# Optimization experiments

Hardware: AMD Instinct MI355X
Metric: run time of the kernel (lower is better)

Reference implementation:

```python
import jax, jax.numpy as jnp
import numpy as np
from jax import lax

T, D, NH, CATS = 1024, 2048, 2048, 1000


def setup_inputs() -> dict:
    key = jax.random.key(0)
    ks = jax.random.split(key, 16)
    s = 0.02
    return {
        "x": jax.random.normal(ks[0], (T, D), dtype=jnp.float32),
        "Wh": jax.random.normal(ks[1], (NH, D), dtype=jnp.float32) * s,
        "Wz": jax.random.normal(ks[2], (NH, D), dtype=jnp.float32) * s,
        "Wr": jax.random.normal(ks[3], (NH, D), dtype=jnp.float32) * s,
        "Uh": jax.random.normal(ks[4], (NH, NH), dtype=jnp.float32) * s,
        "Uz": jax.random.normal(ks[5], (NH, NH), dtype=jnp.float32) * s,
        "bz": jax.random.normal(ks[6], (NH,), dtype=jnp.float32) * s,
        "Ur": jax.random.normal(ks[7], (NH, NH), dtype=jnp.float32) * s,
        "br": jax.random.normal(ks[8], (NH,), dtype=jnp.float32) * s,
        "Wout": jax.random.normal(ks[9], (CATS, NH), dtype=jnp.float32) * s,
        "h0": jax.random.normal(ks[10], (NH,), dtype=jnp.float32),
        "zt0": jax.random.normal(ks[11], (NH,), dtype=jnp.float32),
        "htilde0": jax.random.normal(ks[12], (NH,), dtype=jnp.float32),
        "hprev0": jax.random.normal(ks[13], (NH,), dtype=jnp.float32),
    }


def reference(x, Wh, Wz, Wr, Uh, Uz, bz, Ur, br, Wout, h0, zt0, htilde0, hprev0):
    # Batch the input projections over all timesteps: [T,d] @ [d,nh] -> [T,nh]
    xh = x @ Wh.T
    xz = x @ Wz.T
    xr = x @ Wr.T

    # Faithful to the original update ORDER: h is computed from the *stale*
    # zt/htilde (from the previous iteration), then gates are refreshed.
    # The original's hadamard(a, b) = linear(a, diag(b)) is exactly a * b.
    def step(carry, xs):
        h, zt, htilde, hprev = carry
        xh_t, xz_t, xr_t = xs
        h_new = (1.0 - zt) * hprev + zt * htilde
        zt_new = jax.nn.sigmoid(xz_t + hprev @ Uz.T + bz)
        htilde_new = jnp.tanh(xh_t + hprev @ Uh.T)
        # rt = sigmoid(xr_t + hprev @ Ur.T + br)  # computed in original, never used
        return (h_new, zt_new, htilde_new, h_new), None

    (h_fin, _, _, _), _ = lax.scan(step, (h0, zt0, htilde0, hprev0), (xh, xz, xr))
    logits = h_fin @ Wout.T  # [cats]
    return jax.nn.softmax(logits, axis=0)
```

## Files before the change

### kernel.cpp

```cpp
#include <hip/hip_runtime.h>
#include <math.h>

#define TT  1024
#define DD  2048
#define NHH 2048
#define CC  1000

__global__ __launch_bounds__(256) void k_gemm(const float* __restrict__ X,
                                              const float* __restrict__ Wh,
                                              const float* __restrict__ Wz,
                                              const float* __restrict__ bz,
                                              float* __restrict__ XH,
                                              float* __restrict__ XZ) {
    __shared__ float As[32][68];
    __shared__ float Bs[32][68];
    const int z = blockIdx.z;
    const float* __restrict__ W = z ? Wz : Wh;
    float* __restrict__ OUT = z ? XZ : XH;
    const int n0 = blockIdx.x * 64;
    const int m0 = blockIdx.y * 64;
    const int tid = threadIdx.x;
    const int tx = tid & 15, ty = tid >> 4;
    const int lr = tid >> 2;
    const int lc = (tid & 3) * 8;

    float acc[4][4] = {};
    for (int k0 = 0; k0 < DD; k0 += 32) {
        float4 a0 = *(const float4*)&X[(size_t)(m0 + lr) * DD + k0 + lc];
        float4 a1 = *(const float4*)&X[(size_t)(m0 + lr) * DD + k0 + lc + 4];
        float4 b0 = *(const float4*)&W[(size_t)(n0 + lr) * DD + k0 + lc];
        float4 b1 = *(const float4*)&W[(size_t)(n0 + lr) * DD + k0 + lc + 4];
        As[lc+0][lr]=a0.x; As[lc+1][lr]=a0.y; As[lc+2][lr]=a0.z; As[lc+3][lr]=a0.w;
        As[lc+4][lr]=a1.x; As[lc+5][lr]=a1.y; As[lc+6][lr]=a1.z; As[lc+7][lr]=a1.w;
        Bs[lc+0][lr]=b0.x; Bs[lc+1][lr]=b0.y; Bs[lc+2][lr]=b0.z; Bs[lc+3][lr]=b0.w;
        Bs[lc+4][lr]=b1.x; Bs[lc+5][lr]=b1.y; Bs[lc+6][lr]=b1.z; Bs[lc+7][lr]=b1.w;
        __syncthreads();
#pragma unroll
        for (int kk = 0; kk < 32; ++kk) {
            float4 av = *(const float4*)&As[kk][ty * 4];
            float4 bv = *(const float4*)&Bs[kk][tx * 4];
            acc[0][0] = fmaf(av.x, bv.x, acc[0][0]); acc[0][1] = fmaf(av.x, bv.y, acc[0][1]);
            acc[0][2] = fmaf(av.x, bv.z, acc[0][2]); acc[0][3] = fmaf(av.x, bv.w, acc[0][3]);
            acc[1][0] = fmaf(av.y, bv.x, acc[1][0]); acc[1][1] = fmaf(av.y, bv.y, acc[1][1]);
            acc[1][2] = fmaf(av.y, bv.z, acc[1][2]); acc[1][3] = fmaf(av.y, bv.w, acc[1][3]);
            acc[2][0] = fmaf(av.z, bv.x, acc[2][0]); acc[2][1] = fmaf(av.z, bv.y, acc[2][1]);
            acc[2][2] = fmaf(av.z, bv.z, acc[2][2]); acc[2][3] = fmaf(av.z, bv.w, acc[2][3]);
            acc[3][0] = fmaf(av.w, bv.x, acc[3][0]); acc[3][1] = fmaf(av.w, bv.y, acc[3][1]);
            acc[3][2] = fmaf(av.w, bv.z, acc[3][2]); acc[3][3] = fmaf(av.w, bv.w, acc[3][3]);
        }
        __syncthreads();
    }
    float4 bias = make_float4(0.f, 0.f, 0.f, 0.f);
    if (z) bias = *(const float4*)&bz[n0 + tx * 4];
#pragma unroll
    for (int i = 0; i < 4; ++i) {
        float4 o = make_float4(acc[i][0] + bias.x, acc[i][1] + bias.y,
                               acc[i][2] + bias.z, acc[i][3] + bias.w);
        *(float4*)&OUT[(size_t)(m0 + ty * 4 + i) * NHH + n0 + tx * 4] = o;
    }
}

__global__ __launch_bounds__(256, 1) void k_recur(
    const float* __restrict__ XH, const float* __restrict__ XZ,
    const float* __restrict__ Uh, const float* __restrict__ Uz,
    const float* __restrict__ zt0, const float* __restrict__ ht0,
    const float* __restrict__ hp0,
    unsigned long long* __restrict__ Hbuf) {
    __shared__ float Hs[NHH];
    __shared__ float dot_s[16];
    const int tid  = threadIdx.x;
    const int wave = tid >> 6, lane = tid & 63;
    const int base8 = blockIdx.x * 8;

    const float* __restrict__ Um = (wave < 2) ? Uz : Uh;
    const int r0 = base8 + (wave & 1) * 4;
    float u[4][32];
#pragma unroll
    for (int r = 0; r < 4; ++r) {
        const float* __restrict__ row = Um + (size_t)(r0 + r) * NHH;
#pragma unroll
        for (int c = 0; c < 8; ++c) {
            float4 v = *(const float4*)&row[c * 256 + lane * 4];
            u[r][c*4+0] = v.x; u[r][c*4+1] = v.y; u[r][c*4+2] = v.z; u[r][c*4+3] = v.w;
        }
    }
#pragma unroll
    for (int k = 0; k < 8; ++k) Hs[k * 256 + tid] = hp0[k * 256 + tid];

    float p_cur = 0.f;
    if (tid < 8) {
        float z0 = zt0[base8 + tid], g0 = ht0[base8 + tid], p0 = hp0[base8 + tid];
        p_cur = (1.0f - z0) * p0 + z0 * g0;
        unsigned long long pr = (1ull << 32) | (unsigned long long)__float_as_uint(p_cur);
        __hip_atomic_store(&Hbuf[(size_t)1 * NHH + base8 + tid], pr,
                           __ATOMIC_RELAXED, __HIP_MEMORY_SCOPE_AGENT);
    }
    __syncthreads();

    for (int t = 1; t < TT; ++t) {
        const unsigned long long* __restrict__ src = Hbuf + (size_t)(t & 3) * NHH;
        unsigned long long pv[8];
#pragma unroll
        for (int k = 0; k < 8; ++k)
            pv[k] = __hip_atomic_load(&src[k * 256 + tid], __ATOMIC_RELAXED, __HIP_MEMORY_SCOPE_AGENT);
        float xzv = 0.f, xhv = 0.f;
        if (tid < 8) {
            xzv = XZ[(size_t)(t - 1) * NHH + base8 + tid];
            xhv = XH[(size_t)(t - 1) * NHH + base8 + tid];
        }
        float a0 = 0.f, a1 = 0.f, a2 = 0.f, a3 = 0.f;
#pragma unroll
        for (int c = 0; c < 8; ++c) {
            float4 h4 = *(const float4*)&Hs[c * 256 + lane * 4];
            a0 = fmaf(u[0][c*4+0], h4.x, fmaf(u[0][c*4+1], h4.y, fmaf(u[0][c*4+2], h4.z, fmaf(u[0][c*4+3], h4.w, a0))));
            a1 = fmaf(u[1][c*4+0], h4.x, fmaf(u[1][c*4+1], h4.y, fmaf(u[1][c*4+2], h4.z, fmaf(u[1][c*4+3], h4.w, a1))));
            a2 = fmaf(u[2][c*4+0], h4.x, fmaf(u[2][c*4+1], h4.y, fmaf(u[2][c*4+2], h4.z, fmaf(u[2][c*4+3], h4.w, a2))));
            a3 = fmaf(u[3][c*4+0], h4.x, fmaf(u[3][c*4+1], h4.y, fmaf(u[3][c*4+2], h4.z, fmaf(u[3][c*4+3], h4.w, a3))));
        }
#pragma unroll
        for (int off = 32; off > 0; off >>= 1) {
            a0 += __shfl_xor(a0, off);
            a1 += __shfl_xor(a1, off);
            a2 += __shfl_xor(a2, off);
            a3 += __shfl_xor(a3, off);
        }
        if (lane == 0) {
            int di = ((wave & 1) * 4) + ((wave >> 1) * 8);
            dot_s[di + 0] = a0; dot_s[di + 1] = a1; dot_s[di + 2] = a2; dot_s[di + 3] = a3;
        }
        __syncthreads();
        if (tid < 8) {
            float z = 1.0f / (1.0f + expf(-(xzv + dot_s[tid])));
            float g = tanhf(xhv + dot_s[8 + tid]);
            float pn = (1.0f - z) * p_cur + z * g;
            p_cur = pn;
            unsigned long long pr = ((unsigned long long)(unsigned)(t + 1) << 32)
                                  | (unsigned long long)__float_as_uint(pn);
            __hip_atomic_store(&Hbuf[(size_t)((t + 1) & 3) * NHH + base8 + tid], pr,
                               __ATOMIC_RELAXED, __HIP_MEMORY_SCOPE_AGENT);
        }
        for (;;) {
            unsigned stale = 0;
#pragma unroll
            for (int k = 0; k < 8; ++k)
                if ((unsigned)(pv[k] >> 32) != (unsigned)t) stale |= (1u << k);
            if (!stale) break;
#pragma unroll
            for (int k = 0; k < 8; ++k)
                if (stale & (1u << k))
                    pv[k] = __hip_atomic_load(&src[k * 256 + tid], __ATOMIC_RELAXED, __HIP_MEMORY_SCOPE_AGENT);
        }
#pragma unroll
        for (int k = 0; k < 8; ++k) Hs[k * 256 + tid] = __uint_as_float((unsigned)pv[k]);
        __syncthreads();
    }
}

__global__ __launch_bounds__(256) void k_logits(const unsigned long long* __restrict__ Hbuf,
                                                const float* __restrict__ Wout,
                                                float* __restrict__ lg) {
    __shared__ float Hs[NHH];
    const int tid = threadIdx.x;
    for (int k = tid; k < NHH; k += 256) Hs[k] = __uint_as_float((unsigned)Hbuf[k]);
    __syncthreads();
    const int wave = tid >> 6, lane = tid & 63;
    const int row = blockIdx.x * 4 + wave;
    float a = 0.f;
#pragma unroll
    for (int c = 0; c < 8; ++c) {
        float4 w = *(const float4*)&Wout[(size_t)row * NHH + c * 256 + lane * 4];
        float4 h = *(const float4*)&Hs[c * 256 + lane * 4];
        a = fmaf(w.x, h.x, fmaf(w.y, h.y, fmaf(w.z, h.z, fmaf(w.w, h.w, a))));
    }
#pragma unroll
    for (int off = 32; off > 0; off >>= 1) a += __shfl_xor(a, off);
    if (lane == 0) lg[row] = a;
}

__global__ __launch_bounds__(1024) void k_softmax(const float* __restrict__ lg,
                                                  float* __restrict__ out) {
    const int i = threadIdx.x;
    __shared__ float red[16];
    __shared__ float bc[2];
    float v = (i < CC) ? lg[i] : -3.0e38f;
    float m = v;
#pragma unroll
    for (int off = 32; off > 0; off >>= 1) m = fmaxf(m, __shfl_xor(m, off));
    if ((i & 63) == 0) red[i >> 6] = m;
    __syncthreads();
    if (i == 0) { float mm = red[0]; for (int k = 1; k < 16; ++k) mm = fmaxf(mm, red[k]); bc[0] = mm; }
    __syncthreads();
    float e = (i < CC) ? expf(v - bc[0]) : 0.f;
    float s = e;
#pragma unroll
    for (int off = 32; off > 0; off >>= 1) s += __shfl_xor(s, off);
    if ((i & 63) == 0) red[i >> 6] = s;
    __syncthreads();
    if (i == 0) { float ss = 0.f; for (int k = 0; k < 16; ++k) ss += red[k]; bc[1] = ss; }
    __syncthreads();
    if (i < CC) out[i] = e / bc[1];
}

extern "C" void kernel_launch(void* const* d_in, const int* in_sizes, int n_in,
                              void* d_out, int out_size, void* d_ws, size_t ws_size,
                              hipStream_t stream) {
    const float* x    = (const float*)d_in[0];
    const float* Wh   = (const float*)d_in[1];
    const float* Wz   = (const float*)d_in[2];
    const float* Uh   = (const float*)d_in[4];
    const float* Uz   = (const float*)d_in[5];
    const float* bz   = (const float*)d_in[6];
    const float* Wout = (const float*)d_in[9];
    const float* zt0  = (const float*)d_in[11];
    const float* ht0  = (const float*)d_in[12];
    const float* hp0  = (const float*)d_in[13];
    float* out = (float*)d_out;

    float* XH = (float*)d_ws;
    float* XZ = XH + (size_t)TT * NHH;
    unsigned long long* Hbuf = (unsigned long long*)(XZ + (size_t)TT * NHH);
    float* lg = (float*)(Hbuf + 4 * NHH);

    k_gemm<<<dim3(NHH / 64, TT / 64, 2), dim3(256), 0, stream>>>(x, Wh, Wz, bz, XH, XZ);
    k_recur<<<dim3(256), dim3(256), 0, stream>>>(XH, XZ, Uh, Uz, zt0, ht0, hp0, Hbuf);
    k_logits<<<dim3(250), dim3(256), 0, stream>>>(Hbuf, Wout, lg);
    k_softmax<<<dim3(1), dim3(1024), 0, stream>>>(lg, out);
}
```

Baseline: 2.054 ms.

## Advance the recurrence two timesteps per grid-wide exchange using the lagged-gate dependency

Each new state depends on the previous state and on gates computed from the state two steps back. The recurrent kernel uses this to keep two consecutive hidden states in shared memory and compute both sets of gate dot products in one round, producing two timesteps per cross-block exchange. This halves the number of global spin-wait synchronisations. Blocks also skip polling for their own slice and write it locally, and a tail step handles the final timestep. The cost is twice the FMA and shuffle work per round, more registers and a second shared buffer.

Measured after the change: 2.665 ms. 29.7% more time.

```diff
diff --git a/kernel.cpp b/kernel.cpp
--- a/kernel.cpp
+++ b/kernel.cpp
@@ -66,8 +66,9 @@
     const float* __restrict__ zt0, const float* __restrict__ ht0,
     const float* __restrict__ hp0,
     unsigned long long* __restrict__ Hbuf) {
-    __shared__ float Hs[NHH];
-    __shared__ float dot_s[16];
+    __shared__ float Ha[NHH];
+    __shared__ float Hb[NHH];
+    __shared__ float dot_s[32];
     const int tid  = threadIdx.x;
     const int wave = tid >> 6, lane = tid & 63;
     const int base8 = blockIdx.x * 8;
@@ -84,75 +85,151 @@
             u[r][c*4+0] = v.x; u[r][c*4+1] = v.y; u[r][c*4+2] = v.z; u[r][c*4+3] = v.w;
         }
     }
-#pragma unroll
-    for (int k = 0; k < 8; ++k) Hs[k * 256 + tid] = hp0[k * 256 + tid];
-
+
+    unsigned ownmask = 0;
+#pragma unroll
+    for (int k = 0; k < 8; ++k)
+        if ((unsigned)(k * 256 + tid - base8) < 8u) ownmask |= (1u << k);
+
+#pragma unroll
+    for (int k = 0; k < 8; ++k) {
+        int i = k * 256 + tid;
+        float p0 = hp0[i], z0 = zt0[i], g0 = ht0[i];
+        Ha[i] = p0;
+        Hb[i] = (1.0f - z0) * p0 + z0 * g0;
+    }
     float p_cur = 0.f;
     if (tid < 8) {
-        float z0 = zt0[base8 + tid], g0 = ht0[base8 + tid], p0 = hp0[base8 + tid];
+        float p0 = hp0[base8 + tid], z0 = zt0[base8 + tid], g0 = ht0[base8 + tid];
         p_cur = (1.0f - z0) * p0 + z0 * g0;
-        unsigned long long pr = (1ull << 32) | (unsigned long long)__float_as_uint(p_cur);
-        __hip_atomic_store(&Hbuf[(size_t)1 * NHH + base8 + tid], pr,
-                           __ATOMIC_RELAXED, __HIP_MEMORY_SCOPE_AGENT);
-    }
-    __syncthreads();
-
-    for (int t = 1; t < TT; ++t) {
-        const unsigned long long* __restrict__ src = Hbuf + (size_t)(t & 3) * NHH;
-        unsigned long long pv[8];
-#pragma unroll
-        for (int k = 0; k < 8; ++k)
-            pv[k] = __hip_atomic_load(&src[k * 256 + tid], __ATOMIC_RELAXED, __HIP_MEMORY_SCOPE_AGENT);
-        float xzv = 0.f, xhv = 0.f;
+    }
+    __syncthreads();
+
+    for (int r = 0; r < (TT - 2) / 2; ++r) {
+        const unsigned ta = (unsigned)(2 * r + 2);
+        const unsigned tb = (unsigned)(2 * r + 3);
+        unsigned long long* __restrict__ sa = Hbuf + (size_t)(((r + 1) & 1) * 2) * NHH;
+        unsigned long long* __restrict__ sb = sa + NHH;
+
+        unsigned long long pva[8], pvb[8];
+#pragma unroll
+        for (int k = 0; k < 8; ++k) {
+            pva[k] = __hip_atomic_load(&sa[k * 256 + tid], __ATOMIC_RELAXED, __HIP_MEMORY_SCOPE_AGENT);
+            pvb[k] = __hip_atomic_load(&sb[k * 256 + tid], __ATOMIC_RELAXED, __HIP_MEMORY_SCOPE_AGENT);
+        }
+        float xzA = 0.f, xhA = 0.f, xzB = 0.f, xhB = 0.f;
         if (tid < 8) {
-            xzv = XZ[(size_t)(t - 1) * NHH + base8 + tid];
-            xhv = XH[(size_t)(t - 1) * NHH + base8 + tid];
-        }
-        float a0 = 0.f, a1 = 0.f, a2 = 0.f, a3 = 0.f;
+            xzA = XZ[(size_t)(2 * r    ) * NHH + base8 + tid];
+            xhA = XH[(size_t)(2 * r    ) * NHH + base8 + tid];
+            xzB = XZ[(size_t)(2 * r + 1) * NHH + base8 + tid];
+            xhB = XH[(size_t)(2 * r + 1) * NHH + base8 + tid];
+        }
+
+        float a0=0.f,a1=0.f,a2=0.f,a3=0.f,b0=0.f,b1=0.f,b2=0.f,b3=0.f;
 #pragma unroll
         for (int c = 0; c < 8; ++c) {
-            float4 h4 = *(const float4*)&Hs[c * 256 + lane * 4];
+            float4 h4 = *(const float4*)&Ha[c * 256 + lane * 4];
+            float4 q4 = *(const float4*)&Hb[c * 256 + lane * 4];
             a0 = fmaf(u[0][c*4+0], h4.x, fmaf(u[0][c*4+1], h4.y, fmaf(u[0][c*4+2], h4.z, fmaf(u[0][c*4+3], h4.w, a0))));
             a1 = fmaf(u[1][c*4+0], h4.x, fmaf(u[1][c*4+1], h4.y, fmaf(u[1][c*4+2], h4.z, fmaf(u[1][c*4+3], h4.w, a1))));
             a2 = fmaf(u[2][c*4+0], h4.x, fmaf(u[2][c*4+1], h4.y, fmaf(u[2][c*4+2], h4.z, fmaf(u[2][c*4+3], h4.w, a2))));
             a3 = fmaf(u[3][c*4+0], h4.x, fmaf(u[3][c*4+1], h4.y, fmaf(u[3][c*4+2], h4.z, fmaf(u[3][c*4+3], h4.w, a3))));
+            b0 = fmaf(u[0][c*4+0], q4.x, fmaf(u[0][c*4+1], q4.y, fmaf(u[0][c*4+2], q4.z, fmaf(u[0][c*4+3], q4.w, b0))));
+            b1 = fmaf(u[1][c*4+0], q4.x, fmaf(u[1][c*4+1], q4.y, fmaf(u[1][c*4+2], q4.z, fmaf(u[1][c*4+3], q4.w, b1))));
+            b2 = fmaf(u[2][c*4+0], q4.x, fmaf(u[2][c*4+1], q4.y, fmaf(u[2][c*4+2], q4.z, fmaf(u[2][c*4+3], q4.w, b2))));
+            b3 = fmaf(u[3][c*4+0], q4.x, fmaf(u[3][c*4+1], q4.y, fmaf(u[3][c*4+2], q4.z, fmaf(u[3][c*4+3], q4.w, b3))));
         }
 #pragma unroll
         for (int off = 32; off > 0; off >>= 1) {
-            a0 += __shfl_xor(a0, off);
-            a1 += __shfl_xor(a1, off);
-            a2 += __shfl_xor(a2, off);
-            a3 += __shfl_xor(a3, off);
+            a0 += __shfl_xor(a0, off); a1 += __shfl_xor(a1, off);
+            a2 += __shfl_xor(a2, off); a3 += __shfl_xor(a3, off);
+            b0 += __shfl_xor(b0, off); b1 += __shfl_xor(b1, off);
+            b2 += __shfl_xor(b2, off); b3 += __shfl_xor(b3, off);
         }
         if (lane == 0) {
             int di = ((wave & 1) * 4) + ((wave >> 1) * 8);
             dot_s[di + 0] = a0; dot_s[di + 1] = a1; dot_s[di + 2] = a2; dot_s[di + 3] = a3;
-        }
-        __syncthreads();
+            dot_s[16 + di + 0] = b0; dot_s[16 + di + 1] = b1;
+            dot_s[16 + di + 2] = b2; dot_s[16 + di + 3] = b3;
+        }
+        __syncthreads();
+
+        float pA = 0.f, pB = 0.f;
         if (tid < 8) {
-            float z = 1.0f / (1.0f + expf(-(xzv + dot_s[tid])));
-            float g = tanhf(xhv + dot_s[8 + tid]);
-            float pn = (1.0f - z) * p_cur + z * g;
-            p_cur = pn;
-            unsigned long long pr = ((unsigned long long)(unsigned)(t + 1) << 32)
-                                  | (unsigned long long)__float_as_uint(pn);
-            __hip_atomic_store(&Hbuf[(size_t)((t + 1) & 3) * NHH + base8 + tid], pr,
-                               __ATOMIC_RELAXED, __HIP_MEMORY_SCOPE_AGENT);
-        }
+            float zA = 1.0f / (1.0f + expf(-(xzA + dot_s[tid])));
+            float gA = tanhf(xhA + dot_s[8 + tid]);
+            pA = (1.0f - zA) * p_cur + zA * gA;
+            float zB = 1.0f / (1.0f + expf(-(xzB + dot_s[16 + tid])));
+            float gB = tanhf(xhB + dot_s[24 + tid]);
+            pB = (1.0f - zB) * pA + zB * gB;
+            p_cur = pB;
+            __hip_atomic_store(&sa[base8 + tid],
+                ((unsigned long long)ta << 32) | (unsigned long long)__float_as_uint(pA),
+                __ATOMIC_RELAXED, __HIP_MEMORY_SCOPE_AGENT);
+            __hip_atomic_store(&sb[base8 + tid],
+                ((unsigned long long)tb << 32) | (unsigned long long)__float_as_uint(pB),
+                __ATOMIC_RELAXED, __HIP_MEMORY_SCOPE_AGENT);
+        }
+
         for (;;) {
             unsigned stale = 0;
 #pragma unroll
-            for (int k = 0; k < 8; ++k)
-                if ((unsigned)(pv[k] >> 32) != (unsigned)t) stale |= (1u << k);
+            for (int k = 0; k < 8; ++k) {
+                if (!(ownmask & (1u << k))) {
+                    if ((unsigned)(pva[k] >> 32) != ta) stale |= (1u << k);
+                    if ((unsigned)(pvb[k] >> 32) != tb) stale |= (0x100u << k);
+                }
+            }
             if (!stale) break;
 #pragma unroll
-            for (int k = 0; k < 8; ++k)
+            for (int k = 0; k < 8; ++k) {
                 if (stale & (1u << k))
-                    pv[k] = __hip_atomic_load(&src[k * 256 + tid], __ATOMIC_RELAXED, __HIP_MEMORY_SCOPE_AGENT);
-        }
-#pragma unroll
-        for (int k = 0; k < 8; ++k) Hs[k * 256 + tid] = __uint_as_float((unsigned)pv[k]);
-        __syncthreads();
+                    pva[k] = __hip_atomic_load(&sa[k * 256 + tid], __ATOMIC_RELAXED, __HIP_MEMORY_SCOPE_AGENT);
+                if (stale & (0x100u << k))
+                    pvb[k] = __hip_atomic_load(&sb[k * 256 + tid], __ATOMIC_RELAXED, __HIP_MEMORY_SCOPE_AGENT);
+            }
+        }
+#pragma unroll
+        for (int k = 0; k < 8; ++k) {
+            if (!(ownmask & (1u << k))) {
+                Ha[k * 256 + tid] = __uint_as_float((unsigned)pva[k]);
+                Hb[k * 256 + tid] = __uint_as_float((unsigned)pvb[k]);
+            }
+        }
+        if (tid < 8) { Ha[base8 + tid] = pA; Hb[base8 + tid] = pB; }
+        __syncthreads();
+    }
+
+    {
+        float a0=0.f,a1=0.f,a2=0.f,a3=0.f;
+#pragma unroll
+        for (int c = 0; c < 8; ++c) {
+            float4 h4 = *(const float4*)&Ha[c * 256 + lane * 4];
+            a0 = fmaf(u[0][c*4+0], h4.x, fmaf(u[0][c*4+1], h4.y, fmaf(u[0][c*4+2], h4.z, fmaf(u[0][c*4+3], h4.w, a0))));
+            a1 = fmaf(u[1][c*4+0], h4.x, fmaf(u[1][c*4+1], h4.y, fmaf(u[1][c*4+2], h4.z, fmaf(u[1][c*4+3], h4.w, a1))));
+            a2 = fmaf(u[2][c*4+0], h4.x, fmaf(u[2][c*4+1], h4.y, fmaf(u[2][c*4+2], h4.z, fmaf(u[2][c*4+3], h4.w, a2))));
+            a3 = fmaf(u[3][c*4+0], h4.x, fmaf(u[3][c*4+1], h4.y, fmaf(u[3][c*4+2], h4.z, fmaf(u[3][c*4+3], h4.w, a3))));
+        }
+#pragma unroll
+        for (int off = 32; off > 0; off >>= 1) {
+            a0 += __shfl_xor(a0, off); a1 += __shfl_xor(a1, off);
+            a2 += __shfl_xor(a2, off); a3 += __shfl_xor(a3, off);
+        }
+        if (lane == 0) {
+            int di = ((wave & 1) * 4) + ((wave >> 1) * 8);
+            dot_s[di + 0] = a0; dot_s[di + 1] = a1; dot_s[di + 2] = a2; dot_s[di + 3] = a3;
+        }
+        __syncthreads();
+        if (tid < 8) {
+            float xz = XZ[(size_t)(TT - 2) * NHH + base8 + tid];
+            float xh = XH[(size_t)(TT - 2) * NHH + base8 + tid];
+            float z = 1.0f / (1.0f + expf(-(xz + dot_s[tid])));
+            float g = tanhf(xh + dot_s[8 + tid]);
+            float pn = (1.0f - z) * p_cur + z * g;
+            __hip_atomic_store(&Hbuf[base8 + tid],
+                ((unsigned long long)1024u << 32) | (unsigned long long)__float_as_uint(pn),
+                __ATOMIC_RELAXED, __HIP_MEMORY_SCOPE_AGENT);
+        }
     }
 }
 
```

## Give each wave both gates per element and double-buffer hidden state to drop a barrier

Applied to the files above, without the earlier changes.

The recurrent kernel now runs 128 blocks of 512 threads. Each wave holds the Uz and Uh rows for two hidden elements, so it finishes the gate update itself without sharing partial dots through LDS. That removes one __syncthreads per timestep, and double-buffering the shared hidden vector lets the next step's loads proceed without a second barrier before the matvec. Fewer blocks have to publish and spin-poll the flag-tagged hidden state, at the cost of a larger per-block polling footprint and more waves per CU.

Result: slower. 2.784 ms (+35.5%).

```diff
diff --git a/kernel.cpp b/kernel.cpp
--- a/kernel.cpp
+++ b/kernel.cpp
@@ -60,58 +60,63 @@
     }
 }
 
-__global__ __launch_bounds__(256, 1) void k_recur(
+__global__ __launch_bounds__(512, 1) void k_recur(
     const float* __restrict__ XH, const float* __restrict__ XZ,
     const float* __restrict__ Uh, const float* __restrict__ Uz,
     const float* __restrict__ zt0, const float* __restrict__ ht0,
     const float* __restrict__ hp0,
     unsigned long long* __restrict__ Hbuf) {
-    __shared__ float Hs[NHH];
-    __shared__ float dot_s[16];
+    __shared__ float Hs[2][NHH];
     const int tid  = threadIdx.x;
     const int wave = tid >> 6, lane = tid & 63;
-    const int base8 = blockIdx.x * 8;
-
-    const float* __restrict__ Um = (wave < 2) ? Uz : Uh;
-    const int r0 = base8 + (wave & 1) * 4;
+    const int base16 = blockIdx.x * 16;
+    const int e0 = base16 + 2 * wave;
+
     float u[4][32];
 #pragma unroll
-    for (int r = 0; r < 4; ++r) {
-        const float* __restrict__ row = Um + (size_t)(r0 + r) * NHH;
+    for (int r = 0; r < 2; ++r) {
+        const float* __restrict__ rowz = Uz + (size_t)(e0 + r) * NHH;
+        const float* __restrict__ rowh = Uh + (size_t)(e0 + r) * NHH;
 #pragma unroll
         for (int c = 0; c < 8; ++c) {
-            float4 v = *(const float4*)&row[c * 256 + lane * 4];
-            u[r][c*4+0] = v.x; u[r][c*4+1] = v.y; u[r][c*4+2] = v.z; u[r][c*4+3] = v.w;
-        }
-    }
-#pragma unroll
-    for (int k = 0; k < 8; ++k) Hs[k * 256 + tid] = hp0[k * 256 + tid];
+            float4 vz = *(const float4*)&rowz[c * 256 + lane * 4];
+            float4 vh = *(const float4*)&rowh[c * 256 + lane * 4];
+            u[r][c*4+0]=vz.x; u[r][c*4+1]=vz.y; u[r][c*4+2]=vz.z; u[r][c*4+3]=vz.w;
+            u[2+r][c*4+0]=vh.x; u[2+r][c*4+1]=vh.y; u[2+r][c*4+2]=vh.z; u[2+r][c*4+3]=vh.w;
+        }
+    }
+
+#pragma unroll
+    for (int k = 0; k < 4; ++k) Hs[0][k * 512 + tid] = hp0[k * 512 + tid];
 
     float p_cur = 0.f;
-    if (tid < 8) {
-        float z0 = zt0[base8 + tid], g0 = ht0[base8 + tid], p0 = hp0[base8 + tid];
+    if (lane < 2) {
+        const int e = e0 + lane;
+        float z0 = zt0[e], g0 = ht0[e], p0 = hp0[e];
         p_cur = (1.0f - z0) * p0 + z0 * g0;
-        unsigned long long pr = (1ull << 32) | (unsigned long long)__float_as_uint(p_cur);
-        __hip_atomic_store(&Hbuf[(size_t)1 * NHH + base8 + tid], pr,
-                           __ATOMIC_RELAXED, __HIP_MEMORY_SCOPE_AGENT);
-    }
-    __syncthreads();
-
+        __hip_atomic_store(&Hbuf[(size_t)1 * NHH + e],
+            (1ull << 32) | (unsigned long long)__float_as_uint(p_cur),
+            __ATOMIC_RELAXED, __HIP_MEMORY_SCOPE_AGENT);
+    }
+    __syncthreads();
+
+    int p = 0;
     for (int t = 1; t < TT; ++t) {
         const unsigned long long* __restrict__ src = Hbuf + (size_t)(t & 3) * NHH;
-        unsigned long long pv[8];
-#pragma unroll
-        for (int k = 0; k < 8; ++k)
-            pv[k] = __hip_atomic_load(&src[k * 256 + tid], __ATOMIC_RELAXED, __HIP_MEMORY_SCOPE_AGENT);
+        unsigned long long pv[4];
+#pragma unroll
+        for (int k = 0; k < 4; ++k)
+            pv[k] = __hip_atomic_load(&src[k * 512 + tid], __ATOMIC_RELAXED, __HIP_MEMORY_SCOPE_AGENT);
         float xzv = 0.f, xhv = 0.f;
-        if (tid < 8) {
-            xzv = XZ[(size_t)(t - 1) * NHH + base8 + tid];
-            xhv = XH[(size_t)(t - 1) * NHH + base8 + tid];
-        }
+        if (lane < 2) {
+            xzv = XZ[(size_t)(t - 1) * NHH + e0 + lane];
+            xhv = XH[(size_t)(t - 1) * NHH + e0 + lane];
+        }
+
         float a0 = 0.f, a1 = 0.f, a2 = 0.f, a3 = 0.f;
 #pragma unroll
         for (int c = 0; c < 8; ++c) {
-            float4 h4 = *(const float4*)&Hs[c * 256 + lane * 4];
+            float4 h4 = *(const float4*)&Hs[p][c * 256 + lane * 4];
             a0 = fmaf(u[0][c*4+0], h4.x, fmaf(u[0][c*4+1], h4.y, fmaf(u[0][c*4+2], h4.z, fmaf(u[0][c*4+3], h4.w, a0))));
             a1 = fmaf(u[1][c*4+0], h4.x, fmaf(u[1][c*4+1], h4.y, fmaf(u[1][c*4+2], h4.z, fmaf(u[1][c*4+3], h4.w, a1))));
             a2 = fmaf(u[2][c*4+0], h4.x, fmaf(u[2][c*4+1], h4.y, fmaf(u[2][c*4+2], h4.z, fmaf(u[2][c*4+3], h4.w, a2))));
@@ -119,40 +124,39 @@
         }
 #pragma unroll
         for (int off = 32; off > 0; off >>= 1) {
-            a0 += __shfl_xor(a0, off);
-            a1 += __shfl_xor(a1, off);
-            a2 += __shfl_xor(a2, off);
-            a3 += __shfl_xor(a3, off);
-        }
-        if (lane == 0) {
-            int di = ((wave & 1) * 4) + ((wave >> 1) * 8);
-            dot_s[di + 0] = a0; dot_s[di + 1] = a1; dot_s[di + 2] = a2; dot_s[di + 3] = a3;
-        }
-        __syncthreads();
-        if (tid < 8) {
-            float z = 1.0f / (1.0f + expf(-(xzv + dot_s[tid])));
-            float g = tanhf(xhv + dot_s[8 + tid]);
+            a0 += __shfl_xor(a0, off); a1 += __shfl_xor(a1, off);
+            a2 += __shfl_xor(a2, off); a3 += __shfl_xor(a3, off);
+        }
+        if (lane < 2) {
+            float dz = lane ? a1 : a0;
+            float dh = lane ? a3 : a2;
+            float z = 1.0f / (1.0f + expf(-(xzv + dz)));
+            float g = tanhf(xhv + dh);
             float pn = (1.0f - z) * p_cur + z * g;
             p_cur = pn;
-            unsigned long long pr = ((unsigned long long)(unsigned)(t + 1) << 32)
-                                  | (unsigned long long)__float_as_uint(pn);
-            __hip_atomic_store(&Hbuf[(size_t)((t + 1) & 3) * NHH + base8 + tid], pr,
-                               __ATOMIC_RELAXED, __HIP_MEMORY_SCOPE_AGENT);
-        }
+            __hip_atomic_store(&Hbuf[(size_t)((t + 1) & 3) * NHH + e0 + lane],
+                ((unsigned long long)(unsigned)(t + 1) << 32)
+                    | (unsigned long long)__float_as_uint(pn),
+                __ATOMIC_RELAXED, __HIP_MEMORY_SCOPE_AGENT);
+        }
+        if (t == TT - 1) break;
+
         for (;;) {
             unsigned stale = 0;
 #pragma unroll
-            for (int k = 0; k < 8; ++k)
+            for (int k = 0; k < 4; ++k)
                 if ((unsigned)(pv[k] >> 32) != (unsigned)t) stale |= (1u << k);
             if (!stale) break;
 #pragma unroll
-            for (int k = 0; k < 8; ++k)
+            for (int k = 0; k < 4; ++k)
                 if (stale & (1u << k))
-                    pv[k] = __hip_atomic_load(&src[k * 256 + tid], __ATOMIC_RELAXED, __HIP_MEMORY_SCOPE_AGENT);
-        }
-#pragma unroll
-        for (int k = 0; k < 8; ++k) Hs[k * 256 + tid] = __uint_as_float((unsigned)pv[k]);
+                    pv[k] = __hip_atomic_load(&src[k * 512 + tid], __ATOMIC_RELAXED, __HIP_MEMORY_SCOPE_AGENT);
+        }
+#pragma unroll
+        for (int k = 0; k < 4; ++k)
+            Hs[p ^ 1][k * 512 + tid] = __uint_as_float((unsigned)pv[k]);
         __syncthreads();
+        p ^= 1;
     }
 }
 
@@ -222,7 +226,7 @@
     float* lg = (float*)(Hbuf + 4 * NHH);
 
     k_gemm<<<dim3(NHH / 64, TT / 64, 2), dim3(256), 0, stream>>>(x, Wh, Wz, bz, XH, XZ);
-    k_recur<<<dim3(256), dim3(256), 0, stream>>>(XH, XZ, Uh, Uz, zt0, ht0, hp0, Hbuf);
+    k_recur<<<dim3(128), dim3(512), 0, stream>>>(XH, XZ, Uh, Uz, zt0, ht0, hp0, Hbuf);
     k_logits<<<dim3(250), dim3(256), 0, stream>>>(Hbuf, Wout, lg);
     k_softmax<<<dim3(1), dim3(1024), 0, stream>>>(lg, out);
 }
```
